# Kernel optimization log

Measured on AMD Instinct MI355X. Metric: run time of the kernel, lower is better.

The kernel has to match this reference:

```python
import jax, jax.numpy as jnp
import numpy as np

B, S = 4096, 32
H, NH, HD = 512, 8, 64
NL = 6            # encoder layers
E = 128           # num_experts
CTX = 32          # context_length
LN_EPS = 1e-5


def _ln(x, w, b):
    mu = jnp.mean(x, axis=-1, keepdims=True)
    var = jnp.mean((x - mu) ** 2, axis=-1, keepdims=True)
    return (x - mu) * jax.lax.rsqrt(var + LN_EPS) * w + b


def setup_inputs() -> dict:
    key = jax.random.key(0)
    ks = jax.random.split(key, 20)
    n = lambda k, shape: (jax.random.normal(k, shape, jnp.float32) * 0.02)
    return dict(
        expert_sequence=jax.random.randint(ks[0], (B, S), 0, E),
        layer_id=jax.random.randint(ks[1], (B,), 0, 12),
        expert_table=n(ks[2], (E, H)),
        layer_table=n(ks[3], (12, H)),
        pos_table=n(ks[4], (CTX, H)),
        qkv_w=n(ks[5], (NL, 3 * H, H)), qkv_b=n(ks[6], (NL, 3 * H)),
        out_w=n(ks[7], (NL, H, H)), out_b=n(ks[8], (NL, H)),
        ln1_w=jnp.ones((NL, H)), ln1_b=jnp.zeros((NL, H)),
        ff1_w=n(ks[9], (NL, 2 * H, H)), ff1_b=n(ks[10], (NL, 2 * H)),
        ff2_w=n(ks[11], (NL, H, 2 * H)), ff2_b=n(ks[12], (NL, H)),
        ln2_w=jnp.ones((NL, H)), ln2_b=jnp.zeros((NL, H)),
        head_w=n(ks[13], (NL, E, H)), head_b=n(ks[14], (NL, E)),
        conf_w=n(ks[15], (1, H)), conf_b=jnp.zeros((1,), jnp.float32),
    )


def reference(expert_sequence, layer_id, expert_table, layer_table, pos_table,
              qkv_w, qkv_b, out_w, out_b, ln1_w, ln1_b,
              ff1_w, ff1_b, ff2_w, ff2_b, ln2_w, ln2_b,
              head_w, head_b, conf_w, conf_b):
    Bn, Sn = expert_sequence.shape
    # embedding sum (position defaults to arange % context_length)
    x = (expert_table[expert_sequence]
         + layer_table[layer_id][:, None, :]
         + pos_table[jnp.arange(Sn) % CTX][None, :, :])  # [B,S,H]

    scale = 1.0 / np.float32(np.sqrt(HD))
    for i in range(NL):  # post-norm TransformerEncoderLayer, relu FFN, eval (no dropout)
        qkv = x @ qkv_w[i].T + qkv_b[i]                  # [B,S,3H]
        q, k, v = jnp.split(qkv, 3, axis=-1)
        hview = lambda t: t.reshape(Bn, Sn, NH, HD).transpose(0, 2, 1, 3)
        q, k, v = hview(q), hview(k), hview(v)           # [B,NH,S,HD]
        att = jax.nn.softmax(jnp.einsum('bhqd,bhkd->bhqk', q, k) * scale, axis=-1)
        o = jnp.einsum('bhqk,bhkd->bhqd', att, v).transpose(0, 2, 1, 3).reshape(Bn, Sn, H)
        x = _ln(x + o @ out_w[i].T + out_b[i], ln1_w[i], ln1_b[i])
        ff = jax.nn.relu(x @ ff1_w[i].T + ff1_b[i]) @ ff2_w[i].T + ff2_b[i]
        x = _ln(x + ff, ln2_w[i], ln2_b[i])

    last = x[:, -1, :]                                   # [B,H]
    # head selection: odd layers {1,3,...,11} -> heads 0..5, else fall back to head '1' (idx 0)
    head_idx = jnp.where(layer_id % 2 == 1, (layer_id - 1) // 2, 0)
    prediction = jnp.einsum('bh,beh->be', last, head_w[head_idx]) + head_b[head_idx]
    confidence = jax.nn.sigmoid(last @ conf_w.T + conf_b)  # [B,1]
    return prediction, confidence
```

## Files before the change

### kernel.cpp

```cpp
#include <hip/hip_runtime.h>

typedef __bf16 bf16;
typedef bf16 bf16x8 __attribute__((ext_vector_type(8)));
typedef bf16 bf16x4 __attribute__((ext_vector_type(4)));
typedef float f32x4 __attribute__((ext_vector_type(4)));

#define B_ 4096
#define S_ 32
#define H_ 512
#define NL_ 6
constexpr size_t TOK = (size_t)B_ * S_;

typedef __attribute__((address_space(1))) void* gas_t;
typedef __attribute__((address_space(3))) void* las_t;

__device__ __forceinline__ void async16(bf16* lds, const bf16* g) {
    __builtin_amdgcn_global_load_lds((gas_t)g, (las_t)lds, 16, 0, 0);
}

template<bool RELU>
__global__ __launch_bounds__(256, 2) void gemm_kernel(
    const bf16* __restrict__ A, int lda, const bf16* __restrict__ W,
    const float* __restrict__ bias,
    bf16* C, int N, int K)
{
    __shared__ __align__(16) bf16 As[128 * 64];
    __shared__ __align__(16) bf16 Bs[128 * 64];
    const int tid  = threadIdx.x;
    const int lane = tid & 63, wid = tid >> 6;
    int m_idx, n_idx;
    {
        const int nb = gridDim.x, mgd = gridDim.y;
        if ((mgd & 7) == 0) {
            int id  = blockIdx.y * nb + blockIdx.x;
            int xcd = id & 7, j = id >> 3;
            n_idx = j % nb;
            m_idx = (j / nb) * 8 + xcd;
        } else { m_idx = blockIdx.y; n_idx = blockIdx.x; }
    }
    const int m0 = m_idx << 7, n0 = n_idx << 7;
    const int r = lane & 15, quad = lane >> 4;
    const int wm = (wid & 1) << 6, wn = (wid >> 1) << 6;

    f32x4 acc[4][4];
#pragma unroll
    for (int i = 0; i < 4; ++i)
#pragma unroll
        for (int j = 0; j < 4; ++j) acc[i][j] = {0.f, 0.f, 0.f, 0.f};

    const int nkt = K >> 6;
    for (int kt = 0; kt < nkt; ++kt) {
        const int k0 = kt << 6;
#pragma unroll
        for (int p = 0; p < 4; ++p) {
            int q   = p * 256 + tid;
            int row = q >> 3;
            int cg  = (q & 7) ^ (row & 7);
            async16(&As[(size_t)(p * 256 + wid * 64) * 8],
                    A + (size_t)(m0 + row) * lda + k0 + cg * 8);
            async16(&Bs[(size_t)(p * 256 + wid * 64) * 8],
                    W + (size_t)(n0 + row) * K + k0 + cg * 8);
        }
        __syncthreads();
#pragma unroll
        for (int ks = 0; ks < 2; ++ks) {
            bf16x8 af[4], bfr[4];
#pragma unroll
            for (int mi = 0; mi < 4; ++mi) {
                int row  = wm + mi * 16 + r;
                int slot = (ks * 4 + quad) ^ (row & 7);
                af[mi] = *(const bf16x8*)&As[row * 64 + slot * 8];
            }
#pragma unroll
            for (int ni = 0; ni < 4; ++ni) {
                int row  = wn + ni * 16 + r;
                int slot = (ks * 4 + quad) ^ (row & 7);
                bfr[ni] = *(const bf16x8*)&Bs[row * 64 + slot * 8];
            }
#pragma unroll
            for (int mi = 0; mi < 4; ++mi)
#pragma unroll
                for (int ni = 0; ni < 4; ++ni)
                    acc[mi][ni] = __builtin_amdgcn_mfma_f32_16x16x32_bf16(
                        af[mi], bfr[ni], acc[mi][ni], 0, 0, 0);
        }
        __syncthreads();
    }
#pragma unroll
    for (int ni = 0; ni < 4; ++ni) {
        int col  = n0 + wn + ni * 16 + r;
        float bv = bias[col];
#pragma unroll
        for (int mi = 0; mi < 4; ++mi) {
            int mrow = m0 + wm + mi * 16 + quad * 4;
#pragma unroll
            for (int rr = 0; rr < 4; ++rr) {
                size_t idx = (size_t)(mrow + rr) * N + col;
                float v = acc[mi][ni][rr] + bv;
                if (RELU) v = fmaxf(v, 0.f);
                C[idx] = (bf16)v;
            }
        }
    }
}

__global__ __launch_bounds__(256, 2) void gemm_ln_kernel(
    const bf16* __restrict__ A, int lda, const bf16* __restrict__ W,
    const float* __restrict__ bias, bf16* x,
    const float* __restrict__ lnw, const float* __restrict__ lnb, int K)
{
    __shared__ __align__(16) bf16 As[64 * 64];
    __shared__ __align__(16) bf16 Ws[512 * 64];
    __shared__ float ps[64][4], ps2[64][4];
    const int tid  = threadIdx.x;
    const int lane = tid & 63, wid = tid >> 6;
    const int m0 = blockIdx.x << 6;
    const int r = lane & 15, quad = lane >> 4;
    const int wn = wid << 7;

    f32x4 acc[4][8];
#pragma unroll
    for (int i = 0; i < 4; ++i)
#pragma unroll
        for (int j = 0; j < 8; ++j) acc[i][j] = {0.f, 0.f, 0.f, 0.f};

    const int nkt = K >> 6;
    for (int kt = 0; kt < nkt; ++kt) {
        const int k0 = kt << 6;
#pragma unroll
        for (int p = 0; p < 2; ++p) {
            int q   = p * 256 + tid;
            int row = q >> 3;
            int cg  = (q & 7) ^ (row & 7);
            async16(&As[(size_t)(p * 256 + wid * 64) * 8],
                    A + (size_t)(m0 + row) * lda + k0 + cg * 8);
        }
#pragma unroll
        for (int p = 0; p < 16; ++p) {
            int q   = p * 256 + tid;
            int row = q >> 3;
            int cg  = (q & 7) ^ (row & 7);
            async16(&Ws[(size_t)(p * 256 + wid * 64) * 8],
                    W + (size_t)row * K + k0 + cg * 8);
        }
        __syncthreads();
#pragma unroll
        for (int ks = 0; ks < 2; ++ks) {
            bf16x8 af[4], wf[8];
#pragma unroll
            for (int mi = 0; mi < 4; ++mi) {
                int row  = mi * 16 + r;
                int slot = (ks * 4 + quad) ^ (row & 7);
                af[mi] = *(const bf16x8*)&As[row * 64 + slot * 8];
            }
#pragma unroll
            for (int ni = 0; ni < 8; ++ni) {
                int row  = wn + ni * 16 + r;
                int slot = (ks * 4 + quad) ^ (row & 7);
                wf[ni] = *(const bf16x8*)&Ws[row * 64 + slot * 8];
            }
#pragma unroll
            for (int mi = 0; mi < 4; ++mi)
#pragma unroll
                for (int ni = 0; ni < 8; ++ni)
                    acc[mi][ni] = __builtin_amdgcn_mfma_f32_16x16x32_bf16(
                        af[mi], wf[ni], acc[mi][ni], 0, 0, 0);
        }
        __syncthreads();
    }

#pragma unroll
    for (int mi = 0; mi < 4; ++mi)
#pragma unroll
        for (int rr = 0; rr < 4; ++rr) {
            int row  = mi * 16 + quad * 4 + rr;
            float s = 0.f, s2 = 0.f;
#pragma unroll
            for (int ni = 0; ni < 8; ++ni) {
                int col = wn + ni * 16 + r;
                float v = acc[mi][ni][rr] + bias[col]
                        + (float)x[(size_t)(m0 + row) * H_ + col];
                acc[mi][ni][rr] = v;
                s += v; s2 += v * v;
            }
#pragma unroll
            for (int off = 8; off >= 1; off >>= 1) {
                s  += __shfl_xor(s,  off, 16);
                s2 += __shfl_xor(s2, off, 16);
            }
            if (r == 0) { ps[row][wid] = s; ps2[row][wid] = s2; }
        }
    __syncthreads();

#pragma unroll
    for (int mi = 0; mi < 4; ++mi)
#pragma unroll
        for (int rr = 0; rr < 4; ++rr) {
            int row = mi * 16 + quad * 4 + rr;
            float s  = ps[row][0] + ps[row][1] + ps[row][2] + ps[row][3];
            float s2 = ps2[row][0] + ps2[row][1] + ps2[row][2] + ps2[row][3];
            float mu  = s * (1.f / 512.f);
            float var = s2 * (1.f / 512.f) - mu * mu;
            float inv = rsqrtf(var + 1e-5f);
#pragma unroll
            for (int ni = 0; ni < 8; ++ni) {
                int col = wn + ni * 16 + r;
                float v = (acc[mi][ni][rr] - mu) * inv * lnw[col] + lnb[col];
                x[(size_t)(m0 + row) * H_ + col] = (bf16)v;
            }
        }
}

__global__ __launch_bounds__(256) void attn_kernel(bf16* qkv)
{
    __shared__ __align__(16) bf16 Pl[4][32][40];
    __shared__ float rs[4][32];
    const int tid = threadIdx.x;
    const int lane = tid & 63, wid = tid >> 6;
    const int pair = blockIdx.x * 4 + wid;
    const int b = pair >> 3, h = pair & 7;
    const int r = lane & 15, quad = lane >> 4;
    bf16* base = qkv + (size_t)b * 32 * 1536 + h * 64;

    bf16x8 aq[2][2], bk[2][2];
#pragma unroll
    for (int t = 0; t < 2; ++t)
#pragma unroll
        for (int ks = 0; ks < 2; ++ks) {
            aq[t][ks] = *(const bf16x8*)(base +       (size_t)(t * 16 + r) * 1536 + ks * 32 + quad * 8);
            bk[t][ks] = *(const bf16x8*)(base + 512 + (size_t)(t * 16 + r) * 1536 + ks * 32 + quad * 8);
        }
    f32x4 sc[2][2];
#pragma unroll
    for (int mt = 0; mt < 2; ++mt)
#pragma unroll
        for (int nt = 0; nt < 2; ++nt) sc[mt][nt] = {0.f, 0.f, 0.f, 0.f};
#pragma unroll
    for (int mt = 0; mt < 2; ++mt)
#pragma unroll
        for (int nt = 0; nt < 2; ++nt)
#pragma unroll
            for (int ks = 0; ks < 2; ++ks)
                sc[mt][nt] = __builtin_amdgcn_mfma_f32_16x16x32_bf16(
                    aq[mt][ks], bk[nt][ks], sc[mt][nt], 0, 0, 0);

#pragma unroll
    for (int mt = 0; mt < 2; ++mt)
#pragma unroll
        for (int rr = 0; rr < 4; ++rr) {
            int i = mt * 16 + quad * 4 + rr;
            float v0 = sc[mt][0][rr] * 0.125f;
            float v1 = sc[mt][1][rr] * 0.125f;
            float mx = fmaxf(v0, v1);
#pragma unroll
            for (int off = 8; off >= 1; off >>= 1) mx = fmaxf(mx, __shfl_xor(mx, off, 16));
            float e0 = __expf(v0 - mx), e1 = __expf(v1 - mx);
            float s = e0 + e1;
#pragma unroll
            for (int off = 8; off >= 1; off >>= 1) s += __shfl_xor(s, off, 16);
            Pl[wid][i][r]      = (bf16)e0;
            Pl[wid][i][r + 16] = (bf16)e1;
            if (r == 0) rs[wid][i] = s;
        }
    __syncthreads();

    const bf16* vb = base + 1024;
    bf16x8 av[4];
#pragma unroll
    for (int mt = 0; mt < 4; ++mt)
#pragma unroll
        for (int jj = 0; jj < 8; ++jj)
            av[mt][jj] = vb[(size_t)(quad * 8 + jj) * 1536 + mt * 16 + r];
    bf16x8 bp[2];
#pragma unroll
    for (int nt = 0; nt < 2; ++nt)
        bp[nt] = *(const bf16x8*)&Pl[wid][nt * 16 + r][quad * 8];
    f32x4 oc[4][2];
#pragma unroll
    for (int mt = 0; mt < 4; ++mt)
#pragma unroll
        for (int nt = 0; nt < 2; ++nt) oc[mt][nt] = {0.f, 0.f, 0.f, 0.f};
#pragma unroll
    for (int mt = 0; mt < 4; ++mt)
#pragma unroll
        for (int nt = 0; nt < 2; ++nt)
            oc[mt][nt] = __builtin_amdgcn_mfma_f32_16x16x32_bf16(av[mt], bp[nt], oc[mt][nt], 0, 0, 0);

    float inv0 = 1.f / rs[wid][r];
    float inv1 = 1.f / rs[wid][r + 16];
    bf16* ob = base;
#pragma unroll
    for (int mt = 0; mt < 4; ++mt)
#pragma unroll
        for (int nt = 0; nt < 2; ++nt) {
            int i = nt * 16 + r;
            float invv = nt ? inv1 : inv0;
            bf16x4 pk;
#pragma unroll
            for (int rr = 0; rr < 4; ++rr) pk[rr] = (bf16)(oc[mt][nt][rr] * invv);
            *(bf16x4*)(ob + (size_t)i * 1536 + mt * 16 + quad * 4) = pk;
        }
}

__global__ __launch_bounds__(256) void embed_kernel(
    const int* __restrict__ seq, const int* __restrict__ lid,
    const float* __restrict__ et, const float* __restrict__ lt, const float* __restrict__ pt,
    bf16* __restrict__ x, int t0)
{
    const int lane = threadIdx.x & 63, wid = threadIdx.x >> 6;
    const int rowl = blockIdx.x * 4 + wid;
    const int rowg = t0 + rowl;
    const int b = rowg >> 5, s = rowg & 31;
    const int e = seq[rowg];
    const int l = lid[b];
    const float* pe = et + (size_t)e * H_ + lane * 8;
    const float* pl = lt + (size_t)l * H_ + lane * 8;
    const float* pp = pt + (size_t)s * H_ + lane * 8;
    bf16x8 o8;
#pragma unroll
    for (int j = 0; j < 8; ++j) o8[j] = (bf16)(pe[j] + pl[j] + pp[j]);
    *(bf16x8*)(x + (size_t)rowl * H_ + lane * 8) = o8;
}

__global__ __launch_bounds__(256) void cvt4_kernel(
    const float* __restrict__ a0, bf16* __restrict__ o0, int n0,
    const float* __restrict__ a1, bf16* __restrict__ o1, int n1,
    const float* __restrict__ a2, bf16* __restrict__ o2, int n2,
    const float* __restrict__ a3, bf16* __restrict__ o3, int n3)
{
    int i = blockIdx.x * 256 + threadIdx.x;
    if (i < n0) { o0[i] = (bf16)a0[i]; }
    i -= n0;
    if (i >= 0 && i < n1) { o1[i] = (bf16)a1[i]; }
    i -= n1;
    if (i >= 0 && i < n2) { o2[i] = (bf16)a2[i]; }
    i -= n2;
    if (i >= 0 && i < n3) { o3[i] = (bf16)a3[i]; }
}

__global__ __launch_bounds__(256) void head_kernel(
    const bf16* __restrict__ x, const int* __restrict__ lid,
    const float* __restrict__ hw, const float* __restrict__ hb,
    const float* __restrict__ cw, const float* __restrict__ cb, float* __restrict__ out, int b0)
{
    __shared__ float last[512];
    __shared__ float part[256];
    const int bl = blockIdx.x, tid = threadIdx.x;
    const int b = b0 + bl;
    const size_t row = (size_t)bl * 32 + 31;
    for (int c = tid; c < 512; c += 256) last[c] = (float)x[row * 512 + c];
    __syncthreads();
    int l = lid[b];
    int hidx = (l & 1) ? ((l - 1) >> 1) : 0;
    int e = tid & 127, half = tid >> 7;
    const float* wr = hw + ((size_t)hidx * 128 + e) * 512 + half * 256;
    float s = 0.f;
    for (int k = 0; k < 256; ++k) s += last[half * 256 + k] * wr[k];
    part[tid] = s;
    __syncthreads();
    if (tid < 128) out[(size_t)b * 128 + tid] = part[tid] + part[tid + 128] + hb[hidx * 128 + tid];
    if (tid >= 128 && tid < 192) {
        int ln = tid - 128;
        float cs = 0.f;
#pragma unroll
        for (int k = 0; k < 8; ++k) cs += last[ln * 8 + k] * cw[ln * 8 + k];
#pragma unroll
        for (int off = 32; off >= 1; off >>= 1) cs += __shfl_xor(cs, off, 64);
        if (ln == 0) out[(size_t)B_ * 128 + b] = 1.f / (1.f + __expf(-(cs + cb[0])));
    }
}

extern "C" void kernel_launch(void* const* d_in, const int* in_sizes, int n_in,
                              void* d_out, int out_size, void* d_ws, size_t ws_size,
                              hipStream_t stream)
{
    const int*   seq          = (const int*)d_in[0];
    const int*   lid          = (const int*)d_in[1];
    const float* expert_table = (const float*)d_in[2];
    const float* layer_table  = (const float*)d_in[3];
    const float* pos_table    = (const float*)d_in[4];
    const float* qkv_w        = (const float*)d_in[5];
    const float* qkv_b        = (const float*)d_in[6];
    const float* out_w        = (const float*)d_in[7];
    const float* out_b        = (const float*)d_in[8];
    const float* ln1_w        = (const float*)d_in[9];
    const float* ln1_b        = (const float*)d_in[10];
    const float* ff1_w        = (const float*)d_in[11];
    const float* ff1_b        = (const float*)d_in[12];
    const float* ff2_w        = (const float*)d_in[13];
    const float* ff2_b        = (const float*)d_in[14];
    const float* ln2_w        = (const float*)d_in[15];
    const float* ln2_b        = (const float*)d_in[16];
    const float* head_w       = (const float*)d_in[17];
    const float* head_b       = (const float*)d_in[18];
    const float* conf_w       = (const float*)d_in[19];
    const float* conf_b       = (const float*)d_in[20];
    float* out = (float*)d_out;

    constexpr size_t NWQ = (size_t)NL_ * 1536 * 512;
    constexpr size_t NWO = (size_t)NL_ * 512 * 512;
    constexpr size_t NW1 = (size_t)NL_ * 1024 * 512;
    constexpr size_t NW2 = (size_t)NL_ * 512 * 1024;
    constexpr size_t WELEM = NWQ + NWO + NW1 + NW2;
    int nchunk = 1;
    while (nchunk < 1024) {
        size_t ct = TOK / (size_t)nchunk;
        size_t need = WELEM * 2 + ct * 2048 * 2;
        if (need <= ws_size) break;
        nchunk <<= 1;
    }
    const size_t chunkTok = TOK / (size_t)nchunk;

    bf16* wq = (bf16*)d_ws;
    bf16* wo = wq + NWQ;
    bf16* w1 = wo + NWO;
    bf16* w2 = w1 + NW1;
    bf16* xb = w2 + NW2;
    bf16* qb = xb + chunkTok * 512;

    cvt4_kernel<<<(int)((WELEM + 255) / 256), 256, 0, stream>>>(
        qkv_w, wq, (int)NWQ, out_w, wo, (int)NWO,
        ff1_w, w1, (int)NW1, ff2_w, w2, (int)NW2);

    const int mg = (int)(chunkTok / 128);
    const int lg = (int)(chunkTok / 64);
    for (int c = 0; c < nchunk; ++c) {
        const int t0 = (int)(c * chunkTok);
        embed_kernel<<<(int)(chunkTok / 4), 256, 0, stream>>>(seq, lid, expert_table, layer_table,
                                                              pos_table, xb, t0);
        for (int i = 0; i < NL_; ++i) {
            gemm_kernel<false><<<dim3(12, mg), 256, 0, stream>>>(
                xb, 512, wq + (size_t)i * 1536 * 512, qkv_b + i * 1536, qb, 1536, 512);
            attn_kernel<<<(int)(chunkTok / 16), 256, 0, stream>>>(qb);
            gemm_ln_kernel<<<lg, 256, 0, stream>>>(
                qb, 1536, wo + (size_t)i * 512 * 512, out_b + i * 512, xb,
                ln1_w + i * 512, ln1_b + i * 512, 512);
            gemm_kernel<true><<<dim3(8, mg), 256, 0, stream>>>(
                xb, 512, w1 + (size_t)i * 1024 * 512, ff1_b + i * 1024, qb, 1024, 512);
            gemm_ln_kernel<<<lg, 256, 0, stream>>>(
                qb, 1024, w2 + (size_t)i * 512 * 1024, ff2_b + i * 512, xb,
                ln2_w + i * 512, ln2_b + i * 512, 1024);
        }
        head_kernel<<<(int)(chunkTok / 32), 256, 0, stream>>>(xb, lid, head_w, head_b,
                                                              conf_w, conf_b, out, t0 / 32);
    }
}
```

Baseline: 5.289 ms.

## Compute only the last token in the final encoder layer

```diff
diff --git a/kernel.cpp b/kernel.cpp
--- a/kernel.cpp
+++ b/kernel.cpp
@@ -22,7 +22,7 @@
 __global__ __launch_bounds__(256, 2) void gemm_kernel(
     const bf16* __restrict__ A, int lda, const bf16* __restrict__ W,
     const float* __restrict__ bias,
-    bf16* C, int N, int K)
+    bf16* C, int ldc, int K)
 {
     __shared__ __align__(16) bf16 As[128 * 64];
     __shared__ __align__(16) bf16 Bs[128 * 64];
@@ -95,7 +95,7 @@
             int mrow = m0 + wm + mi * 16 + quad * 4;
 #pragma unroll
             for (int rr = 0; rr < 4; ++rr) {
-                size_t idx = (size_t)(mrow + rr) * N + col;
+                size_t idx = (size_t)(mrow + rr) * ldc + col;
                 float v = acc[mi][ni][rr] + bv;
                 if (RELU) v = fmaxf(v, 0.f);
                 C[idx] = (bf16)v;
@@ -106,7 +106,7 @@
 
 __global__ __launch_bounds__(256, 2) void gemm_ln_kernel(
     const bf16* __restrict__ A, int lda, const bf16* __restrict__ W,
-    const float* __restrict__ bias, bf16* x,
+    const float* __restrict__ bias, bf16* x, int ldx,
     const float* __restrict__ lnw, const float* __restrict__ lnb, int K)
 {
     __shared__ __align__(16) bf16 As[64 * 64];
@@ -179,7 +179,7 @@
             for (int ni = 0; ni < 8; ++ni) {
                 int col = wn + ni * 16 + r;
                 float v = acc[mi][ni][rr] + bias[col]
-                        + (float)x[(size_t)(m0 + row) * H_ + col];
+                        + (float)x[(size_t)(m0 + row) * ldx + col];
                 acc[mi][ni][rr] = v;
                 s += v; s2 += v * v;
             }
@@ -206,7 +206,7 @@
             for (int ni = 0; ni < 8; ++ni) {
                 int col = wn + ni * 16 + r;
                 float v = (acc[mi][ni][rr] - mu) * inv * lnw[col] + lnb[col];
-                x[(size_t)(m0 + row) * H_ + col] = (bf16)v;
+                x[(size_t)(m0 + row) * ldx + col] = (bf16)v;
             }
         }
 }
@@ -300,6 +300,47 @@
             for (int rr = 0; rr < 4; ++rr) pk[rr] = (bf16)(oc[mt][nt][rr] * invv);
             *(bf16x4*)(ob + (size_t)i * 1536 + mt * 16 + quad * 4) = pk;
         }
+}
+
+__global__ __launch_bounds__(256) void attn_last_kernel(bf16* qkv)
+{
+    const int tid = threadIdx.x;
+    const int lane = tid & 63, wid = tid >> 6;
+    const int pair = blockIdx.x * 4 + wid;
+    const int b = pair >> 3, h = pair & 7;
+    bf16* base = qkv + (size_t)b * 32 * 1536 + h * 64;
+    const bf16* qrow = base + 31 * 1536;
+
+    float s;
+    if (lane < 32) {
+        const bf16* krow = base + 512 + (size_t)lane * 1536;
+        float acc = 0.f;
+#pragma unroll
+        for (int d = 0; d < 64; d += 8) {
+            bf16x8 qv = *(const bf16x8*)(qrow + d);
+            bf16x8 kv = *(const bf16x8*)(krow + d);
+#pragma unroll
+            for (int j = 0; j < 8; ++j) acc += (float)qv[j] * (float)kv[j];
+        }
+        s = acc * 0.125f;
+    } else s = -1e30f;
+    float mx = s;
+#pragma unroll
+    for (int off = 16; off >= 1; off >>= 1) mx = fmaxf(mx, __shfl_xor(mx, off, 32));
+    float e = __expf(s - mx);
+    float sum = e;
+#pragma unroll
+    for (int off = 16; off >= 1; off >>= 1) sum += __shfl_xor(sum, off, 32);
+
+    const bf16* vb = base + 1024;
+    float o = 0.f;
+#pragma unroll
+    for (int j = 0; j < 32; ++j) {
+        float pj = __shfl(e, j, 64);
+        o += pj * (float)vb[(size_t)j * 1536 + lane];
+    }
+    float inv = 1.f / __shfl(sum, 0, 64);
+    ((bf16*)base)[31 * 1536 + lane] = (bf16)(o * inv);
 }
 
 __global__ __launch_bounds__(256) void embed_kernel(
@@ -424,22 +465,51 @@
 
     const int mg = (int)(chunkTok / 128);
     const int lg = (int)(chunkTok / 64);
+    const bool fast = (chunkTok % 4096) == 0;
+    const int mL = (int)(chunkTok / 32);
+
     for (int c = 0; c < nchunk; ++c) {
         const int t0 = (int)(c * chunkTok);
         embed_kernel<<<(int)(chunkTok / 4), 256, 0, stream>>>(seq, lid, expert_table, layer_table,
                                                               pos_table, xb, t0);
         for (int i = 0; i < NL_; ++i) {
-            gemm_kernel<false><<<dim3(12, mg), 256, 0, stream>>>(
-                xb, 512, wq + (size_t)i * 1536 * 512, qkv_b + i * 1536, qb, 1536, 512);
-            attn_kernel<<<(int)(chunkTok / 16), 256, 0, stream>>>(qb);
-            gemm_ln_kernel<<<lg, 256, 0, stream>>>(
-                qb, 1536, wo + (size_t)i * 512 * 512, out_b + i * 512, xb,
-                ln1_w + i * 512, ln1_b + i * 512, 512);
-            gemm_kernel<true><<<dim3(8, mg), 256, 0, stream>>>(
-                xb, 512, w1 + (size_t)i * 1024 * 512, ff1_b + i * 1024, qb, 1024, 512);
-            gemm_ln_kernel<<<lg, 256, 0, stream>>>(
-                qb, 1024, w2 + (size_t)i * 512 * 1024, ff2_b + i * 512, xb,
-                ln2_w + i * 512, ln2_b + i * 512, 1024);
+            const bf16* wq_i = wq + (size_t)i * 1536 * 512;
+            const bf16* wo_i = wo + (size_t)i * 512 * 512;
+            const bf16* w1_i = w1 + (size_t)i * 1024 * 512;
+            const bf16* w2_i = w2 + (size_t)i * 512 * 1024;
+            const bool last = fast && (i == NL_ - 1);
+            if (!last) {
+                gemm_kernel<false><<<dim3(12, mg), 256, 0, stream>>>(
+                    xb, 512, wq_i, qkv_b + i * 1536, qb, 1536, 512);
+                attn_kernel<<<(int)(chunkTok / 16), 256, 0, stream>>>(qb);
+                gemm_ln_kernel<<<lg, 256, 0, stream>>>(
+                    qb, 1536, wo_i, out_b + i * 512, xb, 512,
+                    ln1_w + i * 512, ln1_b + i * 512, 512);
+                gemm_kernel<true><<<dim3(8, mg), 256, 0, stream>>>(
+                    xb, 512, w1_i, ff1_b + i * 1024, qb, 1024, 512);
+                gemm_ln_kernel<<<lg, 256, 0, stream>>>(
+                    qb, 1024, w2_i, ff2_b + i * 512, xb, 512,
+                    ln2_w + i * 512, ln2_b + i * 512, 1024);
+            } else {
+                gemm_kernel<false><<<dim3(8, mg), 256, 0, stream>>>(
+                    xb, 512, wq_i + (size_t)512 * 512, qkv_b + i * 1536 + 512,
+                    qb + 512, 1536, 512);
+                gemm_kernel<false><<<dim3(4, mL / 128), 256, 0, stream>>>(
+                    xb + 31 * 512, 32 * 512, wq_i, qkv_b + i * 1536,
+                    qb + (size_t)31 * 1536, 32 * 1536, 512);
+                attn_last_kernel<<<(int)(chunkTok / 16), 256, 0, stream>>>(qb);
+                gemm_ln_kernel<<<mL / 64, 256, 0, stream>>>(
+                    qb + (size_t)31 * 1536, 32 * 1536, wo_i, out_b + i * 512,
+                    xb + 31 * 512, 32 * 512,
+                    ln1_w + i * 512, ln1_b + i * 512, 512);
+                gemm_kernel<true><<<dim3(8, mL / 128), 256, 0, stream>>>(
+                    xb + 31 * 512, 32 * 512, w1_i, ff1_b + i * 1024,
+                    qb + (size_t)31 * 1536, 32 * 1536, 512);
+                gemm_ln_kernel<<<mL / 64, 256, 0, stream>>>(
+                    qb + (size_t)31 * 1536, 32 * 1536, w2_i, ff2_b + i * 512,
+                    xb + 31 * 512, 32 * 512,
+                    ln2_w + i * 512, ln2_b + i * 512, 1024);
+            }
         }
         head_kernel<<<(int)(chunkTok / 32), 256, 0, stream>>>(xb, lid, head_w, head_b,
                                                               conf_w, conf_b, out, t0 / 32);
```

Result: faster. 4.987 ms (-5.7%).
